# Kernel optimization log

Measured on AMD Instinct MI355X. Metric: run time of the kernel, lower is better.

The kernel has to match this reference:

```python
import jax, jax.numpy as jnp
import numpy as np
import math

B, S = 2, 2048
IN_FEATURES = 4096
OUT_FEATURES = 4096
BLOCK_SIZE = 64
NUM_FFT_MATRICES = 4
IN_BLOCKS = IN_FEATURES // BLOCK_SIZE
OUT_BLOCKS = OUT_FEATURES // BLOCK_SIZE  # 64


def setup_inputs() -> dict:
    key = jax.random.key(0)
    k1, k2 = jax.random.split(key)
    scale = 1.0 / math.sqrt(BLOCK_SIZE * IN_BLOCKS)
    x = jax.random.normal(k1, (B, S, IN_FEATURES), dtype=jnp.float32)
    circulant_params = jax.random.normal(
        k2, (NUM_FFT_MATRICES, OUT_BLOCKS, IN_BLOCKS, BLOCK_SIZE), dtype=jnp.float32) * scale
    channel_weights = jnp.ones((NUM_FFT_MATRICES,), dtype=jnp.float32) / NUM_FFT_MATRICES
    return {"x": x, "circulant_params": circulant_params, "channel_weights": channel_weights}


def reference(x, circulant_params, channel_weights):
    b, s, in_feat = x.shape
    # split channels into circulant blocks: (b, s, in_blocks, block)
    x_blocks = x.reshape(b, s, IN_BLOCKS, BLOCK_SIZE)
    x_fft = jnp.fft.rfft(x_blocks, axis=-1)                    # (b, s, i, F) complex
    circ_fft = jnp.fft.rfft(circulant_params, axis=-1)         # (m, o, i, F) complex
    # channel-weighted combine over the m fft matrices (linear, so fold into weights)
    circ_w = jnp.einsum('m,moif->oif', channel_weights.astype(circ_fft.dtype), circ_fft)
    # per-frequency complex contraction over in_blocks (the block-circulant matmul)
    y_fft = jnp.einsum('bsif,oif->bsof', x_fft, circ_w)        # (b, s, o, F)
    y = jnp.fft.irfft(y_fft, n=BLOCK_SIZE, axis=-1)            # (b, s, o, block)
    return y.reshape(b, s, OUT_FEATURES).astype(x.dtype)
```

## Files before the change

kernel.cpp:

```cpp
#include <hip/hip_runtime.h>
#include <math.h>


typedef unsigned short u16;
typedef unsigned int   u32;
typedef __attribute__((ext_vector_type(8))) short bf16x8;
typedef __attribute__((ext_vector_type(4))) float f32x4;

#define TWO_PI 6.2831853071795864769f

#define SF 2056
#define BF_ELEMS (33u*128u*128u)
#define DT_OFF   BF_ELEMS
#define DT_ELEMS (2u*4u*80u*8u)
#define E_OFF    (DT_OFF + DT_ELEMS)
#define E_ELEMS  (3u*4u*64u*8u)

__device__ __forceinline__ u16 f2bf(float f) {
    union { float f; unsigned u; } v; v.f = f;
    unsigned r = v.u + 0x7FFFu + ((v.u >> 16) & 1u);
    return (u16)(r >> 16);
}

__global__ void prep(const float* __restrict__ p, const float* __restrict__ cw,
                     u16* __restrict__ Bf, u16* __restrict__ Dt, u16* __restrict__ E) {
    const int tid = threadIdx.x;
    if (blockIdx.x == 0) {
        for (int e = tid; e < (int)DT_ELEMS; e += 256) {
            int j = e & 7, rowid = e >> 3;
            int n = rowid % 80, grp = rowid / 80;
            int k = (grp >> 2) * 32 + (grp & 3) * 8 + j;
            float v = 0.f;
            if (n < 66) {
                int f = n >> 1;
                float ang = TWO_PI * (float)((f * k) & 63) * (1.f / 64.f);
                v = (n & 1) ? -sinf(ang) : cosf(ang);
            }
            Dt[e] = f2bf(v);
        }
        for (int e = tid; e < (int)E_ELEMS; e += 256) {
            int j = e & 7, rowid = e >> 3;
            int t = rowid % 64, grp = rowid / 64;
            int k = (grp >> 2) * 32 + (grp & 3) * 8 + j;
            float v = 0.f;
            if (k < 66) {
                int f = k >> 1;
                float wf = (f == 0 || f == 32) ? 1.f : 2.f;
                float ang = TWO_PI * (float)((f * t) & 63) * (1.f / 64.f);
                v = (wf * (1.f / 64.f)) * ((k & 1) ? -sinf(ang) : cosf(ang));
            }
            E[e] = f2bf(v);
        }
        return;
    }
    __shared__ float  ct[4][64];
    __shared__ float2 trig[64];
    const int pr = tid >> 6, ln = tid & 63;
    if (tid < 64) {
        float s, c;
        sincosf(TWO_PI * (float)tid * (1.f / 64.f), &s, &c);
        trig[tid] = make_float2(s, c);
    }
    const int pg = (blockIdx.x - 1) * 4 + pr;
    const int o = pg >> 6, i = pg & 63;
    {
        const float* base = p + (size_t)o * 4096 + i * 64 + ln;
        ct[pr][ln] = cw[0] * base[0]      + cw[1] * base[262144]
                   + cw[2] * base[524288] + cw[3] * base[786432];
    }
    __syncthreads();
    if (ln < 33) {
        float cr = 0.f, ci = 0.f;
        for (int u = 0; u < 64; ++u) {
            float2 sc = trig[(ln * u) & 63];
            cr += ct[pr][u] * sc.y; ci -= ct[pr][u] * sc.x;
        }
        u16* b = Bf + (size_t)ln * 16384 + (2 * o) * 128 + 2 * i;
        b[0]   = f2bf(cr);  b[1]   = f2bf(-ci);
        b[128] = f2bf(ci);  b[129] = f2bf(cr);
    }
}

__global__ __launch_bounds__(512) void fused(const float* __restrict__ x,
                                             const u16* __restrict__ Dt,
                                             const u16* __restrict__ Bf,
                                             const u16* __restrict__ E2,
                                             float* __restrict__ y) {
    __shared__ u16 sm[33 * SF];
    const int tid = threadIdx.x, lane = tid & 63, wave = tid >> 6;
    const int lm = lane & 15, q = lane >> 4, kq8 = q * 8, r0 = q * 4;
    const float* xb = x + (size_t)blockIdx.x * (16u * 4096u);

#pragma unroll
    for (int pass = 0; pass < 2; ++pass) {
        f32x4 acc[4][5];
#pragma unroll
        for (int mi = 0; mi < 4; ++mi)
#pragma unroll
            for (int ni = 0; ni < 5; ++ni) acc[mi][ni] = (f32x4){0.f,0.f,0.f,0.f};
#pragma unroll
        for (int kt = 0; kt < 2; ++kt) {
            bf16x8 bfr[5];
#pragma unroll
            for (int ni = 0; ni < 5; ++ni)
                bfr[ni] = *(const bf16x8*)&Dt[((kt*4 + q)*80 + ni*16 + lm)*8];
#pragma unroll
            for (int mi = 0; mi < 4; ++mi) {
                const int row = wave*128 + pass*64 + mi*16 + lm;
                const float* rp = xb + row*64 + kt*32 + kq8;
                float4 p0 = *(const float4*)rp;
                float4 p1 = *(const float4*)(rp + 4);
                union { u16 u[8]; bf16x8 v; } pk;
                pk.u[0]=f2bf(p0.x); pk.u[1]=f2bf(p0.y);
                pk.u[2]=f2bf(p0.z); pk.u[3]=f2bf(p0.w);
                pk.u[4]=f2bf(p1.x); pk.u[5]=f2bf(p1.y);
                pk.u[6]=f2bf(p1.z); pk.u[7]=f2bf(p1.w);
#pragma unroll
                for (int ni = 0; ni < 5; ++ni)
                    acc[mi][ni] = __builtin_amdgcn_mfma_f32_16x16x32_bf16(
                        pk.v, bfr[ni], acc[mi][ni], 0, 0, 0);
            }
        }
#pragma unroll
        for (int mi = 0; mi < 4; ++mi)
#pragma unroll
            for (int ni = 0; ni < 5; ++ni) {
                const int col = ni*16 + lm;
                if (col < 66) {
                    const int f = col >> 1, par = col & 1;
                    const int mb = wave*128 + pass*64 + mi*16 + r0;
                    f32x4 v = acc[mi][ni];
#pragma unroll
                    for (int r = 0; r < 4; ++r) {
                        int m = mb + r, tok = m >> 6, ii = m & 63;
                        sm[f*SF + tok*128 + (((ii<<1)|par) ^ ((tok&7)<<3))] = f2bf(v[r]);
                    }
                }
            }
    }
    __syncthreads();

    for (int f = wave; f < 33; f += 8) {
        u16* sl = &sm[f * SF];
        const u16* Bff = Bf + (size_t)f * 16384;
        bf16x8 af[4];
#pragma unroll
        for (int ks = 0; ks < 4; ++ks)
            af[ks] = *(const bf16x8*)&sl[lm*128 + ((ks*32 + kq8) ^ ((lm&7)<<3))];
#pragma unroll
        for (int nt = 0; nt < 8; ++nt) {
            f32x4 c = (f32x4){0.f,0.f,0.f,0.f};
#pragma unroll
            for (int ks = 0; ks < 4; ++ks) {
                bf16x8 bq = *(const bf16x8*)&Bff[(nt*16 + lm)*128 + ks*32 + kq8];
                c = __builtin_amdgcn_mfma_f32_16x16x32_bf16(af[ks], bq, c, 0, 0, 0);
            }
#pragma unroll
            for (int r = 0; r < 4; ++r) {
                int tok = r0 + r;
                sl[tok*128 + ((nt*16 + lm) ^ ((tok&7)<<3))] = f2bf(c[r]);
            }
        }
    }
    __syncthreads();

    bf16x8 ef[3][4];
#pragma unroll
    for (int kt = 0; kt < 3; ++kt)
#pragma unroll
        for (int mt = 0; mt < 4; ++mt)
            ef[kt][mt] = *(const bf16x8*)&E2[((kt*4 + q)*64 + mt*16 + lm)*8];
#pragma unroll
    for (int nt = 0; nt < 8; ++nt) {
        const int tokL = wave*2 + (nt >> 2);
        const int o = (nt & 3)*16 + lm;
        const int cb = tokL*128 + ((2*o) ^ ((tokL&7)<<3));
        f32x4 acc[4];
#pragma unroll
        for (int mt = 0; mt < 4; ++mt) acc[mt] = (f32x4){0.f,0.f,0.f,0.f};
#pragma unroll
        for (int kt = 0; kt < 3; ++kt) {
            union { u32 w[4]; bf16x8 v; } bq;
#pragma unroll
            for (int j = 0; j < 4; ++j) {
                int f = kt*16 + q*4 + j;
                u32 vv = 0u;
                if (f < 33) vv = *(const u32*)&sm[f*SF + cb];
                bq.w[j] = vv;
            }
#pragma unroll
            for (int mt = 0; mt < 4; ++mt)
                acc[mt] = __builtin_amdgcn_mfma_f32_16x16x32_bf16(
                    ef[kt][mt], bq.v, acc[mt], 0, 0, 0);
        }
        float* yb = y + ((size_t)(blockIdx.x*16 + tokL))*4096 + o*64;
#pragma unroll
        for (int mt = 0; mt < 4; ++mt) {
            float4 st = { acc[mt][0], acc[mt][1], acc[mt][2], acc[mt][3] };
            *(float4*)&yb[mt*16 + r0] = st;
        }
    }
}

extern "C" void kernel_launch(void* const* d_in, const int* in_sizes, int n_in,
                              void* d_out, int out_size, void* d_ws, size_t ws_size,
                              hipStream_t stream) {
    const float* x      = (const float*)d_in[0];
    const float* params = (const float*)d_in[1];
    const float* cw     = (const float*)d_in[2];
    float* out = (float*)d_out;

    u16* Bf = (u16*)d_ws;
    u16* Dt = Bf + DT_OFF;
    u16* Eg = Bf + E_OFF;

    prep<<<1025, 256, 0, stream>>>(params, cw, Bf, Dt, Eg);
    fused<<<256, 512, 0, stream>>>(x, Dt, Bf, Eg, out);
}
```

Baseline: 161.7 us.

## Software-pipeline x loads and Bf fragments, balance frequency-33 work across waves

Stage 1 now loads the second pass's x rows before scattering the first pass's results, so global load latency overlaps LDS writes. Stage 2 double-buffers the Bf fragments per n-tile so the next loads are issued before the current MFMAs. The leftover 33rd frequency is split across all 8 waves (one n-tile each) instead of being done by a single wave, with an extra barrier added to protect its slice. Launch bounds now request 2 blocks per CU, and the E fragments are hoisted earlier; together these raise register pressure and risk spills.

New measurement: 161.7 us. Within noise of the previous version (+0.0%).

```diff
diff --git a/kernel.cpp b/kernel.cpp
--- a/kernel.cpp
+++ b/kernel.cpp
@@ -81,95 +81,142 @@
     }
 }
 
-__global__ __launch_bounds__(512) void fused(const float* __restrict__ x,
-                                             const u16* __restrict__ Dt,
-                                             const u16* __restrict__ Bf,
-                                             const u16* __restrict__ E2,
-                                             float* __restrict__ y) {
+__global__ __launch_bounds__(512, 2) void fused(const float* __restrict__ x,
+                                                const u16* __restrict__ Dt,
+                                                const u16* __restrict__ Bf,
+                                                const u16* __restrict__ E2,
+                                                float* __restrict__ y) {
     __shared__ u16 sm[33 * SF];
     const int tid = threadIdx.x, lane = tid & 63, wave = tid >> 6;
     const int lm = lane & 15, q = lane >> 4, kq8 = q * 8, r0 = q * 4;
     const float* xb = x + (size_t)blockIdx.x * (16u * 4096u);
 
-#pragma unroll
-    for (int pass = 0; pass < 2; ++pass) {
+#define LOADX(XV, pass)                                                      \
+    _Pragma("unroll") for (int kt = 0; kt < 2; ++kt)                         \
+    _Pragma("unroll") for (int mi = 0; mi < 4; ++mi) {                       \
+        const float* rp = xb + (wave*128 + (pass)*64 + mi*16 + lm)*64        \
+                             + kt*32 + kq8;                                  \
+        XV[kt][mi][0] = *(const float4*)rp;                                  \
+        XV[kt][mi][1] = *(const float4*)(rp + 4);                            \
+    }
+#define MFMAPASS(XV, ACC)                                                    \
+    _Pragma("unroll") for (int kt = 0; kt < 2; ++kt)                         \
+    _Pragma("unroll") for (int mi = 0; mi < 4; ++mi) {                       \
+        union { u16 u[8]; bf16x8 v; } pk;                                    \
+        float4 p0 = XV[kt][mi][0], p1 = XV[kt][mi][1];                       \
+        pk.u[0]=f2bf(p0.x); pk.u[1]=f2bf(p0.y);                              \
+        pk.u[2]=f2bf(p0.z); pk.u[3]=f2bf(p0.w);                              \
+        pk.u[4]=f2bf(p1.x); pk.u[5]=f2bf(p1.y);                              \
+        pk.u[6]=f2bf(p1.z); pk.u[7]=f2bf(p1.w);                              \
+        _Pragma("unroll") for (int ni = 0; ni < 5; ++ni)                     \
+            ACC[mi][ni] = __builtin_amdgcn_mfma_f32_16x16x32_bf16(           \
+                pk.v, bfr[kt][ni], ACC[mi][ni], 0, 0, 0);                    \
+    }
+#define SCATTER(ACC, pass)                                                   \
+    {                                                                        \
+        const int tok = wave*2 + (pass);                                     \
+        const int sw  = (tok & 7) << 3;                                      \
+        _Pragma("unroll") for (int mi = 0; mi < 4; ++mi)                     \
+        _Pragma("unroll") for (int ni = 0; ni < 5; ++ni) {                   \
+            const int col = ni*16 + lm;                                      \
+            if (col < 66) {                                                  \
+                const int f = col >> 1, par = col & 1;                       \
+                f32x4 v = ACC[mi][ni];                                       \
+                _Pragma("unroll") for (int r = 0; r < 4; ++r) {              \
+                    int ii = mi*16 + r0 + r;                                 \
+                    sm[f*SF + tok*128 + (((ii<<1)|par) ^ sw)] = f2bf(v[r]);  \
+                }                                                            \
+            }                                                                \
+        }                                                                    \
+    }
+    {
+        float4 xv0[2][4][2];
+        LOADX(xv0, 0)
+        bf16x8 bfr[2][5];
+#pragma unroll
+        for (int kt = 0; kt < 2; ++kt)
+#pragma unroll
+            for (int ni = 0; ni < 5; ++ni)
+                bfr[kt][ni] = *(const bf16x8*)&Dt[((kt*4 + q)*80 + ni*16 + lm)*8];
         f32x4 acc[4][5];
 #pragma unroll
         for (int mi = 0; mi < 4; ++mi)
 #pragma unroll
             for (int ni = 0; ni < 5; ++ni) acc[mi][ni] = (f32x4){0.f,0.f,0.f,0.f};
-#pragma unroll
-        for (int kt = 0; kt < 2; ++kt) {
-            bf16x8 bfr[5];
-#pragma unroll
-            for (int ni = 0; ni < 5; ++ni)
-                bfr[ni] = *(const bf16x8*)&Dt[((kt*4 + q)*80 + ni*16 + lm)*8];
-#pragma unroll
-            for (int mi = 0; mi < 4; ++mi) {
-                const int row = wave*128 + pass*64 + mi*16 + lm;
-                const float* rp = xb + row*64 + kt*32 + kq8;
-                float4 p0 = *(const float4*)rp;
-                float4 p1 = *(const float4*)(rp + 4);
-                union { u16 u[8]; bf16x8 v; } pk;
-                pk.u[0]=f2bf(p0.x); pk.u[1]=f2bf(p0.y);
-                pk.u[2]=f2bf(p0.z); pk.u[3]=f2bf(p0.w);
-                pk.u[4]=f2bf(p1.x); pk.u[5]=f2bf(p1.y);
-                pk.u[6]=f2bf(p1.z); pk.u[7]=f2bf(p1.w);
-#pragma unroll
-                for (int ni = 0; ni < 5; ++ni)
-                    acc[mi][ni] = __builtin_amdgcn_mfma_f32_16x16x32_bf16(
-                        pk.v, bfr[ni], acc[mi][ni], 0, 0, 0);
-            }
-        }
+        MFMAPASS(xv0, acc)
+        float4 xv1[2][4][2];
+        LOADX(xv1, 1)
+        SCATTER(acc, 0)
 #pragma unroll
         for (int mi = 0; mi < 4; ++mi)
 #pragma unroll
-            for (int ni = 0; ni < 5; ++ni) {
-                const int col = ni*16 + lm;
-                if (col < 66) {
-                    const int f = col >> 1, par = col & 1;
-                    const int mb = wave*128 + pass*64 + mi*16 + r0;
-                    f32x4 v = acc[mi][ni];
-#pragma unroll
-                    for (int r = 0; r < 4; ++r) {
-                        int m = mb + r, tok = m >> 6, ii = m & 63;
-                        sm[f*SF + tok*128 + (((ii<<1)|par) ^ ((tok&7)<<3))] = f2bf(v[r]);
-                    }
-                }
-            }
-    }
-    __syncthreads();
-
-    for (int f = wave; f < 33; f += 8) {
+            for (int ni = 0; ni < 5; ++ni) acc[mi][ni] = (f32x4){0.f,0.f,0.f,0.f};
+        MFMAPASS(xv1, acc)
+        SCATTER(acc, 1)
+    }
+    __syncthreads();
+
+    bf16x8 ef[3][4];
+#pragma unroll
+    for (int kt = 0; kt < 3; ++kt)
+#pragma unroll
+        for (int mt = 0; mt < 4; ++mt)
+            ef[kt][mt] = *(const bf16x8*)&E2[((kt*4 + q)*64 + mt*16 + lm)*8];
+
+    bf16x8 af32[4], bq32[4];
+#pragma unroll
+    for (int ks = 0; ks < 4; ++ks)
+        af32[ks] = *(const bf16x8*)&sm[32*SF + lm*128 + ((ks*32 + kq8) ^ ((lm&7)<<3))];
+#pragma unroll
+    for (int ks = 0; ks < 4; ++ks)
+        bq32[ks] = *(const bf16x8*)&Bf[(size_t)32*16384 + (wave*16 + lm)*128 + ks*32 + kq8];
+    __syncthreads();
+
+#pragma unroll
+    for (int t = 0; t < 4; ++t) {
+        const int f = t*8 + wave;
         u16* sl = &sm[f * SF];
         const u16* Bff = Bf + (size_t)f * 16384;
         bf16x8 af[4];
 #pragma unroll
         for (int ks = 0; ks < 4; ++ks)
             af[ks] = *(const bf16x8*)&sl[lm*128 + ((ks*32 + kq8) ^ ((lm&7)<<3))];
+        bf16x8 bc[4], bn[4];
+#pragma unroll
+        for (int ks = 0; ks < 4; ++ks)
+            bc[ks] = *(const bf16x8*)&Bff[lm*128 + ks*32 + kq8];
 #pragma unroll
         for (int nt = 0; nt < 8; ++nt) {
+            if (nt < 7)
+#pragma unroll
+                for (int ks = 0; ks < 4; ++ks)
+                    bn[ks] = *(const bf16x8*)&Bff[((nt+1)*16 + lm)*128 + ks*32 + kq8];
             f32x4 c = (f32x4){0.f,0.f,0.f,0.f};
 #pragma unroll
-            for (int ks = 0; ks < 4; ++ks) {
-                bf16x8 bq = *(const bf16x8*)&Bff[(nt*16 + lm)*128 + ks*32 + kq8];
-                c = __builtin_amdgcn_mfma_f32_16x16x32_bf16(af[ks], bq, c, 0, 0, 0);
-            }
+            for (int ks = 0; ks < 4; ++ks)
+                c = __builtin_amdgcn_mfma_f32_16x16x32_bf16(af[ks], bc[ks], c, 0, 0, 0);
 #pragma unroll
             for (int r = 0; r < 4; ++r) {
                 int tok = r0 + r;
                 sl[tok*128 + ((nt*16 + lm) ^ ((tok&7)<<3))] = f2bf(c[r]);
             }
-        }
-    }
-    __syncthreads();
-
-    bf16x8 ef[3][4];
-#pragma unroll
-    for (int kt = 0; kt < 3; ++kt)
-#pragma unroll
-        for (int mt = 0; mt < 4; ++mt)
-            ef[kt][mt] = *(const bf16x8*)&E2[((kt*4 + q)*64 + mt*16 + lm)*8];
+#pragma unroll
+            for (int ks = 0; ks < 4; ++ks) bc[ks] = bn[ks];
+        }
+    }
+    {
+        f32x4 c = (f32x4){0.f,0.f,0.f,0.f};
+#pragma unroll
+        for (int ks = 0; ks < 4; ++ks)
+            c = __builtin_amdgcn_mfma_f32_16x16x32_bf16(af32[ks], bq32[ks], c, 0, 0, 0);
+#pragma unroll
+        for (int r = 0; r < 4; ++r) {
+            int tok = r0 + r;
+            sm[32*SF + tok*128 + ((wave*16 + lm) ^ ((tok&7)<<3))] = f2bf(c[r]);
+        }
+    }
+    __syncthreads();
+
 #pragma unroll
     for (int nt = 0; nt < 8; ++nt) {
         const int tokL = wave*2 + (nt >> 2);
```

## Fuse circulant weight prep into main kernel via cooperative grid sync

Applied to the files above, without the earlier changes.

Merges the separate prep kernel into the main kernel, which now runs as a cooperative launch. Each block computes 16 of the circulant block FFTs into the shared Bf workspace and then waits on a grid-wide barrier before the frequency-domain contraction. The DFT and inverse-DFT bf16 fragments are now built in registers from a shared trig table instead of being loaded from global memory. This removes one kernel launch and its gap, but adds the cost of a grid sync and relies on all 256 large-LDS blocks being co-resident.

Result: slower. 259.6 us (+60.5%).

```diff
diff --git a/kernel.cpp b/kernel.cpp
--- a/kernel.cpp
+++ b/kernel.cpp
@@ -1,6 +1,9 @@
 #include <hip/hip_runtime.h>
+#include <hip/hip_cooperative_groups.h>
 #include <math.h>
 
+
+namespace cg = cooperative_groups;
 
 typedef unsigned short u16;
 typedef unsigned int   u32;
@@ -8,13 +11,7 @@
 typedef __attribute__((ext_vector_type(4))) float f32x4;
 
 #define TWO_PI 6.2831853071795864769f
-
 #define SF 2056
-#define BF_ELEMS (33u*128u*128u)
-#define DT_OFF   BF_ELEMS
-#define DT_ELEMS (2u*4u*80u*8u)
-#define E_OFF    (DT_OFF + DT_ELEMS)
-#define E_ELEMS  (3u*4u*64u*8u)
 
 __device__ __forceinline__ u16 f2bf(float f) {
     union { float f; unsigned u; } v; v.f = f;
@@ -22,74 +19,70 @@
     return (u16)(r >> 16);
 }
 
-__global__ void prep(const float* __restrict__ p, const float* __restrict__ cw,
-                     u16* __restrict__ Bf, u16* __restrict__ Dt, u16* __restrict__ E) {
-    const int tid = threadIdx.x;
-    if (blockIdx.x == 0) {
-        for (int e = tid; e < (int)DT_ELEMS; e += 256) {
-            int j = e & 7, rowid = e >> 3;
-            int n = rowid % 80, grp = rowid / 80;
-            int k = (grp >> 2) * 32 + (grp & 3) * 8 + j;
-            float v = 0.f;
-            if (n < 66) {
-                int f = n >> 1;
-                float ang = TWO_PI * (float)((f * k) & 63) * (1.f / 64.f);
-                v = (n & 1) ? -sinf(ang) : cosf(ang);
-            }
-            Dt[e] = f2bf(v);
-        }
-        for (int e = tid; e < (int)E_ELEMS; e += 256) {
-            int j = e & 7, rowid = e >> 3;
-            int t = rowid % 64, grp = rowid / 64;
-            int k = (grp >> 2) * 32 + (grp & 3) * 8 + j;
-            float v = 0.f;
-            if (k < 66) {
-                int f = k >> 1;
-                float wf = (f == 0 || f == 32) ? 1.f : 2.f;
-                float ang = TWO_PI * (float)((f * t) & 63) * (1.f / 64.f);
-                v = (wf * (1.f / 64.f)) * ((k & 1) ? -sinf(ang) : cosf(ang));
-            }
-            E[e] = f2bf(v);
-        }
-        return;
-    }
-    __shared__ float  ct[4][64];
+__global__ __launch_bounds__(512) void fused_all(const float* __restrict__ x,
+                                                 const float* __restrict__ p,
+                                                 const float* __restrict__ cw,
+                                                 u16* __restrict__ Bf,
+                                                 float* __restrict__ y) {
+    __shared__ u16    sm[33 * SF];
     __shared__ float2 trig[64];
-    const int pr = tid >> 6, ln = tid & 63;
+    __shared__ float  ctw[8][2][64];
+    const int tid = threadIdx.x, lane = tid & 63, wave = tid >> 6;
+    const int lm = lane & 15, q = lane >> 4, kq8 = q * 8, r0 = q * 4;
+    const float* xb = x + (size_t)blockIdx.x * 65536u;
+
     if (tid < 64) {
         float s, c;
         sincosf(TWO_PI * (float)tid * (1.f / 64.f), &s, &c);
         trig[tid] = make_float2(s, c);
     }
-    const int pg = (blockIdx.x - 1) * 4 + pr;
-    const int o = pg >> 6, i = pg & 63;
-    {
-        const float* base = p + (size_t)o * 4096 + i * 64 + ln;
-        ct[pr][ln] = cw[0] * base[0]      + cw[1] * base[262144]
-                   + cw[2] * base[524288] + cw[3] * base[786432];
-    }
     __syncthreads();
-    if (ln < 33) {
-        float cr = 0.f, ci = 0.f;
-        for (int u = 0; u < 64; ++u) {
-            float2 sc = trig[(ln * u) & 63];
-            cr += ct[pr][u] * sc.y; ci -= ct[pr][u] * sc.x;
-        }
-        u16* b = Bf + (size_t)ln * 16384 + (2 * o) * 128 + 2 * i;
-        b[0]   = f2bf(cr);  b[1]   = f2bf(-ci);
-        b[128] = f2bf(ci);  b[129] = f2bf(cr);
-    }
-}
-
-__global__ __launch_bounds__(512) void fused(const float* __restrict__ x,
-                                             const u16* __restrict__ Dt,
-                                             const u16* __restrict__ Bf,
-                                             const u16* __restrict__ E2,
-                                             float* __restrict__ y) {
-    __shared__ u16 sm[33 * SF];
-    const int tid = threadIdx.x, lane = tid & 63, wave = tid >> 6;
-    const int lm = lane & 15, q = lane >> 4, kq8 = q * 8, r0 = q * 4;
-    const float* xb = x + (size_t)blockIdx.x * (16u * 4096u);
+
+#pragma unroll
+    for (int p2 = 0; p2 < 2; ++p2) {
+        const int pg = blockIdx.x * 16 + wave * 2 + p2;
+        const int o = pg >> 6, i = pg & 63;
+        const float* base = p + (size_t)o * 4096 + i * 64 + lane;
+        ctw[wave][p2][lane] = cw[0] * base[0]      + cw[1] * base[262144]
+                            + cw[2] * base[524288] + cw[3] * base[786432];
+    }
+    __syncthreads();
+#pragma unroll
+    for (int p2 = 0; p2 < 2; ++p2) {
+        const int pg = blockIdx.x * 16 + wave * 2 + p2;
+        const int o = pg >> 6, i = pg & 63;
+        if (lane < 33) {
+            float cr = 0.f, ci = 0.f;
+            for (int u = 0; u < 64; ++u) {
+                float2 sc = trig[(lane * u) & 63];
+                float t = ctw[wave][p2][u];
+                cr += t * sc.y; ci -= t * sc.x;
+            }
+            u16* b = Bf + (size_t)lane * 16384 + (2 * o) * 128 + 2 * i;
+            b[0]   = f2bf(cr);  b[1]   = f2bf(-ci);
+            b[128] = f2bf(ci);  b[129] = f2bf(cr);
+        }
+    }
+
+    bf16x8 bfr[2][5];
+#pragma unroll
+    for (int kt = 0; kt < 2; ++kt)
+#pragma unroll
+        for (int ni = 0; ni < 5; ++ni) {
+            const int n = ni * 16 + lm, f = n >> 1, par = n & 1;
+            union { u16 u[8]; bf16x8 v; } pk;
+#pragma unroll
+            for (int j = 0; j < 8; ++j) {
+                const int k = kt * 32 + kq8 + j;
+                float v = 0.f;
+                if (n < 66) {
+                    float2 sc = trig[(f * k) & 63];
+                    v = par ? -sc.x : sc.y;
+                }
+                pk.u[j] = f2bf(v);
+            }
+            bfr[kt][ni] = pk.v;
+        }
 
 #pragma unroll
     for (int pass = 0; pass < 2; ++pass) {
@@ -100,10 +93,6 @@
             for (int ni = 0; ni < 5; ++ni) acc[mi][ni] = (f32x4){0.f,0.f,0.f,0.f};
 #pragma unroll
         for (int kt = 0; kt < 2; ++kt) {
-            bf16x8 bfr[5];
-#pragma unroll
-            for (int ni = 0; ni < 5; ++ni)
-                bfr[ni] = *(const bf16x8*)&Dt[((kt*4 + q)*80 + ni*16 + lm)*8];
 #pragma unroll
             for (int mi = 0; mi < 4; ++mi) {
                 const int row = wave*128 + pass*64 + mi*16 + lm;
@@ -118,9 +107,11 @@
 #pragma unroll
                 for (int ni = 0; ni < 5; ++ni)
                     acc[mi][ni] = __builtin_amdgcn_mfma_f32_16x16x32_bf16(
-                        pk.v, bfr[ni], acc[mi][ni], 0, 0, 0);
-            }
-        }
+                        pk.v, bfr[kt][ni], acc[mi][ni], 0, 0, 0);
+            }
+        }
+        const int tok = wave*2 + pass;
+        const int sw  = (tok & 7) << 3;
 #pragma unroll
         for (int mi = 0; mi < 4; ++mi)
 #pragma unroll
@@ -128,17 +119,18 @@
                 const int col = ni*16 + lm;
                 if (col < 66) {
                     const int f = col >> 1, par = col & 1;
-                    const int mb = wave*128 + pass*64 + mi*16 + r0;
                     f32x4 v = acc[mi][ni];
 #pragma unroll
                     for (int r = 0; r < 4; ++r) {
-                        int m = mb + r, tok = m >> 6, ii = m & 63;
-                        sm[f*SF + tok*128 + (((ii<<1)|par) ^ ((tok&7)<<3))] = f2bf(v[r]);
+                        int ii = mi*16 + r0 + r;
+                        sm[f*SF + tok*128 + (((ii<<1)|par) ^ sw)] = f2bf(v[r]);
                     }
                 }
             }
     }
-    __syncthreads();
+
+    __threadfence();
+    cg::this_grid().sync();
 
     for (int f = wave; f < 33; f += 8) {
         u16* sl = &sm[f * SF];
@@ -168,8 +160,23 @@
 #pragma unroll
     for (int kt = 0; kt < 3; ++kt)
 #pragma unroll
-        for (int mt = 0; mt < 4; ++mt)
-            ef[kt][mt] = *(const bf16x8*)&E2[((kt*4 + q)*64 + mt*16 + lm)*8];
+        for (int mt = 0; mt < 4; ++mt) {
+            const int t = mt * 16 + lm;
+            union { u16 u[8]; bf16x8 v; } pk;
+#pragma unroll
+            for (int j = 0; j < 8; ++j) {
+                const int k = kt * 32 + kq8 + j;
+                float v = 0.f;
+                if (k < 66) {
+                    const int f = k >> 1;
+                    const float wf = (f == 0 || f == 32) ? 1.f : 2.f;
+                    float2 sc = trig[(f * t) & 63];
+                    v = (wf * (1.f / 64.f)) * ((k & 1) ? -sc.x : sc.y);
+                }
+                pk.u[j] = f2bf(v);
+            }
+            ef[kt][mt] = pk.v;
+        }
 #pragma unroll
     for (int nt = 0; nt < 8; ++nt) {
         const int tokL = wave*2 + (nt >> 2);
@@ -209,11 +216,10 @@
     const float* params = (const float*)d_in[1];
     const float* cw     = (const float*)d_in[2];
     float* out = (float*)d_out;
-
     u16* Bf = (u16*)d_ws;
-    u16* Dt = Bf + DT_OFF;
-    u16* Eg = Bf + E_OFF;
-
-    prep<<<1025, 256, 0, stream>>>(params, cw, Bf, Dt, Eg);
-    fused<<<256, 512, 0, stream>>>(x, Dt, Bf, Eg, out);
+
+    void* args[] = { (void*)&x, (void*)&params, (void*)&cw,
+                     (void*)&Bf, (void*)&out };
+    hipLaunchCooperativeKernel((const void*)fused_all, dim3(256), dim3(512),
+                               args, 0, stream);
 }
```
